# Kernel optimization log

Hardware: AMD Instinct MI355X
Metric: run time of the kernel (lower is better)

Reference implementation:

```python
import jax, jax.numpy as jnp
import numpy as np

B, C, H, W = 8, 512, 64, 64
CQ = C // 8  # query/key projection dim


def setup_inputs() -> dict:
    key = jax.random.key(0)
    ks = jax.random.split(key, 8)
    s = 0.02
    return {
        "x": jax.random.normal(ks[0], (B, C, H, W), dtype=jnp.float32),
        "Wq": jax.random.normal(ks[1], (CQ, C), dtype=jnp.float32) * s,
        "bq": jax.random.normal(ks[2], (CQ,), dtype=jnp.float32) * s,
        "Wk": jax.random.normal(ks[3], (CQ, C), dtype=jnp.float32) * s,
        "bk": jax.random.normal(ks[4], (CQ,), dtype=jnp.float32) * s,
        "Wv": jax.random.normal(ks[5], (C, C), dtype=jnp.float32) * s,
        "bv": jax.random.normal(ks[6], (C,), dtype=jnp.float32) * s,
        "gamma": jax.random.normal(ks[7], (1,), dtype=jnp.float32) * 0.1,
    }


def reference(x, Wq, bq, Wk, bk, Wv, bv, gamma):
    b, c, h, w = x.shape
    n = h * w
    xf = x.reshape(b, c, n)                                  # [B,C,N]
    # 1x1 convs == per-pixel linear maps over channels
    q = jnp.einsum('dc,bcn->bdn', Wq, xf) + bq[:, None]       # [B,CQ,N]
    k = jnp.einsum('dc,bcn->bdn', Wk, xf) + bk[:, None]       # [B,CQ,N]
    v = jnp.einsum('dc,bcn->bdn', Wv, xf) + bv[:, None]       # [B,C,N]
    # attention[b, i, j] = softmax_j( q_i . k_j )
    attn = jax.nn.softmax(jnp.einsum('bdn,bdm->bnm', q, k), axis=-1)  # [B,N,N]
    # out[b, c, i] = sum_j v[b, c, j] * attn[b, i, j]
    out = jnp.einsum('bcj,bij->bci', v, attn).reshape(b, c, h, w)
    return gamma[0] * out + x
```

## Files before the change

kernel.cpp:

```cpp
#include <hip/hip_runtime.h>
#include <hip/hip_bf16.h>

#define BB 8
#define CC 512
#define NN 4096
#define CQ 64

typedef __bf16 bf16;
typedef __bf16 bf16x4 __attribute__((ext_vector_type(4)));
typedef __bf16 bf16x8 __attribute__((ext_vector_type(8)));
typedef float f32x4 __attribute__((ext_vector_type(4)));

__device__ __forceinline__ f32x4 mfma16(bf16x8 a, bf16x8 b, f32x4 c) {
    return __builtin_amdgcn_mfma_f32_16x16x32_bf16(a, b, c, 0, 0, 0);
}

#define BAR_LDS()                                            \
    do {                                                     \
        asm volatile("s_waitcnt lgkmcnt(0)" ::: "memory");   \
        __builtin_amdgcn_s_barrier();                        \
    } while (0)


__global__ __launch_bounds__(256) void k_transpose(const float* __restrict__ x,
                                                   bf16* __restrict__ xTt) {
    __shared__ float tile[64][65];
    const int b  = blockIdx.z;
    const int c0 = blockIdx.y * 64;
    const int n0 = blockIdx.x * 64;
    const int t  = threadIdx.x;

    const float* xp = x + ((size_t)b * CC + c0) * NN + n0;
#pragma unroll
    for (int r = 0; r < 16; ++r) {
        int c = r * 4 + (t >> 6);
        int n = t & 63;
        tile[c][n] = xp[(size_t)c * NN + n];
    }
    __syncthreads();
#pragma unroll
    for (int r = 0; r < 16; ++r) {
        int nl = r * 4 + (t >> 6);
        int cl = t & 63;
        size_t off = ((size_t)(b * 256 + (n0 >> 4) + (nl >> 4)) * 16 + (c0 >> 5) + (cl >> 5)) * 512
                   + (nl & 15) * 32 + (cl & 31);
        xTt[off] = (bf16)tile[cl][nl];
    }
}

__global__ __launch_bounds__(256) void k_castw(const float* __restrict__ Wq,
                                               const float* __restrict__ Wk,
                                               const float* __restrict__ Wv,
                                               bf16* __restrict__ Wqt,
                                               bf16* __restrict__ Wkt,
                                               bf16* __restrict__ Wvt) {
    int i = blockIdx.x * 256 + threadIdx.x;
    const int nqk = CQ * CC;
    const float* src;
    bf16* dst;
    int j;
    if (i < nqk) {
        src = Wq; dst = Wqt; j = i;
    } else if (i < 2 * nqk) {
        src = Wk; dst = Wkt; j = i - nqk;
    } else if (i < 2 * nqk + CC * CC) {
        src = Wv; dst = Wvt; j = i - 2 * nqk;
    } else {
        return;
    }
    int d = j >> 9;
    int c = j & 511;
    size_t off = ((size_t)(d >> 4) * 16 + (c >> 5)) * 512 + (d & 15) * 32 + (c & 31);
    dst[off] = (bf16)src[j];
}

__global__ __launch_bounds__(256) void k_proj_qk(const bf16* __restrict__ xTt,
                                                 const bf16* __restrict__ Wqt,
                                                 const bf16* __restrict__ Wkt,
                                                 const float* __restrict__ bq,
                                                 const float* __restrict__ bk,
                                                 bf16* __restrict__ qTt,
                                                 bf16* __restrict__ kTt) {
    const int b  = blockIdx.y;
    const int nt = blockIdx.x * 4 + (threadIdx.x >> 6);
    const int l  = threadIdx.x & 63;
    const int l15 = l & 15, lq = l >> 4;
    const int loff = l15 * 32 + lq * 8;

    f32x4 acc[8];
#pragma unroll
    for (int dt = 0; dt < 4; ++dt) {
        float bvq = bq[dt * 16 + l15];
        float bvk = bk[dt * 16 + l15];
        acc[dt]     = (f32x4){bvq, bvq, bvq, bvq};
        acc[4 + dt] = (f32x4){bvk, bvk, bvk, bvk};
    }

    const bf16* ap = xTt + ((size_t)(b * 256 + nt) * 16) * 512 + loff;
#pragma unroll 2
    for (int ct = 0; ct < 16; ++ct) {
        bf16x8 a = *(const bf16x8*)(ap + (size_t)ct * 512);
#pragma unroll
        for (int dt = 0; dt < 4; ++dt) {
            bf16x8 fq = *(const bf16x8*)(Wqt + ((size_t)dt * 16 + ct) * 512 + loff);
            acc[dt] = mfma16(a, fq, acc[dt]);
        }
#pragma unroll
        for (int dt = 0; dt < 4; ++dt) {
            bf16x8 fk = *(const bf16x8*)(Wkt + ((size_t)dt * 16 + ct) * 512 + loff);
            acc[4 + dt] = mfma16(a, fk, acc[4 + dt]);
        }
    }
#pragma unroll
    for (int dt = 0; dt < 4; ++dt) {
#pragma unroll
        for (int r = 0; r < 4; ++r) {
            size_t off = ((size_t)(b * 256 + nt) * 2 + (dt >> 1)) * 512
                       + (lq * 4 + r) * 32 + (dt & 1) * 16 + l15;
            qTt[off] = (bf16)acc[dt][r];
            kTt[off] = (bf16)acc[4 + dt][r];
        }
    }
}

__global__ __launch_bounds__(256, 2) void k_proj_v(const bf16* __restrict__ xTt,
                                                   const bf16* __restrict__ Wvt,
                                                   const float* __restrict__ bv,
                                                   bf16* __restrict__ vt) {
    const int b  = blockIdx.y;
    const int bx = blockIdx.x;
    const int w  = threadIdx.x >> 6;
    const int l  = threadIdx.x & 63;
    const int l15 = l & 15, lq = l >> 4;
    const int loff = l15 * 32 + lq * 8;

    f32x4 acc[8][4];
#pragma unroll
    for (int dt = 0; dt < 8; ++dt) {
        f32x4 binit;
#pragma unroll
        for (int r = 0; r < 4; ++r) binit[r] = bv[(w * 8 + dt) * 16 + lq * 4 + r];
#pragma unroll
        for (int nt = 0; nt < 4; ++nt) acc[dt][nt] = binit;
    }

    const bf16* ap = Wvt + ((size_t)(w * 8) * 16) * 512 + loff;
    const bf16* bp = xTt + ((size_t)(b * 256 + bx * 4) * 16) * 512 + loff;
#pragma unroll 1
    for (int ct = 0; ct < 16; ++ct) {
        bf16x8 bxf[4];
#pragma unroll
        for (int nt = 0; nt < 4; ++nt)
            bxf[nt] = *(const bf16x8*)(bp + ((size_t)nt * 16 + ct) * 512);
#pragma unroll
        for (int dt = 0; dt < 8; ++dt) {
            bf16x8 aW = *(const bf16x8*)(ap + ((size_t)dt * 16 + ct) * 512);
#pragma unroll
            for (int nt = 0; nt < 4; ++nt)
                acc[dt][nt] = mfma16(aW, bxf[nt], acc[dt][nt]);
        }
    }
#pragma unroll
    for (int dt = 0; dt < 8; ++dt) {
#pragma unroll
        for (int nt = 0; nt < 4; ++nt) {
#pragma unroll
            for (int r = 0; r < 4; ++r) {
                size_t off = ((size_t)(b * 32 + w * 8 + dt) * 128 + bx * 2 + (nt >> 1)) * 512
                           + (lq * 4 + r) * 32 + (nt & 1) * 16 + l15;
                vt[off] = (bf16)acc[dt][nt][r];
            }
        }
    }
}

__global__ __launch_bounds__(512, 2) void k_attn(const bf16* __restrict__ qTt,
                                                 const bf16* __restrict__ kTt,
                                                 const bf16* __restrict__ vt,
                                                 const float* __restrict__ x,
                                                 const float* __restrict__ gamma,
                                                 float* __restrict__ out) {
    __shared__ bf16  Pl[2][8][1024];
    __shared__ bf16  Kl[2][8][512];
    __shared__ float Ll[8][16];

    const int b  = blockIdx.x & 7;
    const int i0 = (blockIdx.x >> 3) * 128;
    const int t  = threadIdx.x;
    const int w  = t >> 6;
    const int l  = t & 63;
    const int l15 = l & 15, lq = l >> 4;
    const int loff = l15 * 32 + lq * 8;

    const f32x4 zero4 = {0.f, 0.f, 0.f, 0.f};

    const bf16* kb = kTt + (size_t)b * 256 * 2 * 512;
    const bf16* qb = qTt + (size_t)b * 256 * 2 * 512;
    const bf16* vb = vt + ((size_t)b * 32 + w * 4) * 128 * 512 + loff;

    bf16x8 qa0, qa1;
    {
        const bf16* qp = qb + ((size_t)((i0 >> 4) + w) * 2) * 512 + loff;
        qa0 = *(const bf16x8*)qp;
        qa1 = *(const bf16x8*)(qp + 512);
    }

    f32x4 acc[4][8];
#pragma unroll
    for (int ct = 0; ct < 4; ++ct)
#pragma unroll
        for (int it = 0; it < 8; ++it) acc[ct][it] = zero4;
    float lsum = 0.f;

    bf16x8 kcur;
    {
        bf16x8 k0 = *(const bf16x8*)(kb + (size_t)w * 512 + loff);
        *(bf16x8*)&Kl[0][w][l * 8] = k0;
        kcur = *(const bf16x8*)(kb + (size_t)(8 + w) * 512 + loff);
    }
    BAR_LDS();

#pragma unroll 2
    for (int jb = 0; jb < NN / 64; ++jb) {
        const int buf = jb & 1;

        bf16x8 va[4][2];
#pragma unroll
        for (int ct = 0; ct < 4; ++ct)
#pragma unroll
            for (int h = 0; h < 2; ++h)
                va[ct][h] = *(const bf16x8*)(vb + ((size_t)ct * 128 + jb * 2 + h) * 512);

        bf16x8 knxt;
        {
            const int jk = (jb + 2) & (NN / 64 - 1);
            knxt = *(const bf16x8*)(kb + ((size_t)jk * 8 + w) * 512 + loff);
        }

        bf16x8 ka[8];
#pragma unroll
        for (int q = 0; q < 8; ++q)
            ka[q] = *(const bf16x8*)&Kl[buf][q][l * 8];

        f32x4 st[4];
#pragma unroll
        for (int jt = 0; jt < 4; ++jt) {
            f32x4 s = mfma16(ka[jt * 2], qa0, zero4);
            st[jt] = mfma16(ka[jt * 2 + 1], qa1, s);
        }

        *(bf16x8*)&Kl[buf ^ 1][w][l * 8] = kcur;
        kcur = knxt;

#pragma unroll
        for (int jt = 0; jt < 4; ++jt) {
            float p0 = __expf(st[jt][0]);
            float p1 = __expf(st[jt][1]);
            float p2 = __expf(st[jt][2]);
            float p3 = __expf(st[jt][3]);
            lsum += (p0 + p1) + (p2 + p3);
            bf16x4 pk = {(bf16)p0, (bf16)p1, (bf16)p2, (bf16)p3};
            int g = jt * 2 + (lq >> 1);
            *(bf16x4*)&Pl[buf][w][g * 128 + l15 * 8 + (lq & 1) * 4] = pk;
        }

        BAR_LDS();

        __builtin_amdgcn_s_setprio(1);
        bf16x8 pA = *(const bf16x8*)&Pl[buf][0][l * 8];
        bf16x8 pB = *(const bf16x8*)&Pl[buf][0][512 + l * 8];
#pragma unroll
        for (int it = 0; it < 8; ++it) {
            bf16x8 nA, nB;
            if (it < 7) {
                nA = *(const bf16x8*)&Pl[buf][it + 1][l * 8];
                nB = *(const bf16x8*)&Pl[buf][it + 1][512 + l * 8];
            }
            acc[0][it] = mfma16(va[0][0], pA, acc[0][it]);
            acc[1][it] = mfma16(va[1][0], pA, acc[1][it]);
            acc[2][it] = mfma16(va[2][0], pA, acc[2][it]);
            acc[3][it] = mfma16(va[3][0], pA, acc[3][it]);
            acc[0][it] = mfma16(va[0][1], pB, acc[0][it]);
            acc[1][it] = mfma16(va[1][1], pB, acc[1][it]);
            acc[2][it] = mfma16(va[2][1], pB, acc[2][it]);
            acc[3][it] = mfma16(va[3][1], pB, acc[3][it]);
            pA = nA;
            pB = nB;
        }
        __builtin_amdgcn_s_setprio(0);
    }

    lsum += __shfl_xor(lsum, 16);
    lsum += __shfl_xor(lsum, 32);
    if (l < 16) Ll[w][l] = lsum;
    __syncthreads();

    const float g = gamma[0];
    float linv[8];
#pragma unroll
    for (int it = 0; it < 8; ++it) linv[it] = 1.0f / Ll[it][l15];

#pragma unroll
    for (int ct = 0; ct < 4; ++ct) {
#pragma unroll
        for (int it = 0; it < 8; ++it) {
#pragma unroll
            for (int r = 0; r < 4; ++r) {
                int c = (w * 4 + ct) * 16 + lq * 4 + r;
                size_t idx = ((size_t)b * CC + c) * NN + i0 + it * 16 + l15;
                out[idx] = g * (acc[ct][it][r] * linv[it]) + x[idx];
            }
        }
    }
}

extern "C" void kernel_launch(void* const* d_in, const int* in_sizes, int n_in,
                              void* d_out, int out_size, void* d_ws, size_t ws_size,
                              hipStream_t stream) {
    const float* x     = (const float*)d_in[0];
    const float* Wq    = (const float*)d_in[1];
    const float* bq    = (const float*)d_in[2];
    const float* Wk    = (const float*)d_in[3];
    const float* bk    = (const float*)d_in[4];
    const float* Wv    = (const float*)d_in[5];
    const float* bv    = (const float*)d_in[6];
    const float* gamma = (const float*)d_in[7];
    float* out = (float*)d_out;

    char* p = (char*)d_ws;
    bf16* xTt = (bf16*)p; p += (size_t)BB * NN * CC * sizeof(bf16);
    bf16* qTt = (bf16*)p; p += (size_t)BB * NN * CQ * sizeof(bf16);
    bf16* kTt = (bf16*)p; p += (size_t)BB * NN * CQ * sizeof(bf16);
    bf16* vt  = (bf16*)p; p += (size_t)BB * CC * NN * sizeof(bf16);
    bf16* Wqt = (bf16*)p; p += (size_t)CQ * CC * sizeof(bf16);
    bf16* Wkt = (bf16*)p; p += (size_t)CQ * CC * sizeof(bf16);
    bf16* Wvt = (bf16*)p; p += (size_t)CC * CC * sizeof(bf16);

    k_transpose<<<dim3(NN / 64, CC / 64, BB), 256, 0, stream>>>(x, xTt);
    k_castw<<<(2 * CQ * CC + CC * CC + 255) / 256, 256, 0, stream>>>(Wq, Wk, Wv, Wqt, Wkt, Wvt);
    k_proj_qk<<<dim3(NN / 64, BB), 256, 0, stream>>>(xTt, Wqt, Wkt, bq, bk, qTt, kTt);
    k_proj_v<<<dim3(NN / 64, BB), 256, 0, stream>>>(xTt, Wvt, bv, vt);
    k_attn<<<256, 512, 0, stream>>>(qTt, kTt, vt, x, gamma, out);
}
```

Before: 211.4 us.

## Software-pipeline QK^T and exp one tile ahead, overlapping with PV MFMAs

Restructures the main attention loop so the scores and exponentials for the next key tile are computed inside the current PV MFMA loop, with a prologue handling the first tile. Each iteration now stores previously computed probabilities to LDS, issues a single barrier, then interleaves exp work with the value-probability MFMAs. This aims to hide the transcendental and LDS write latency behind matrix-core work. It drops the unroll-by-2, removes the software prefetch of P rows, and raises register pressure by keeping packed probabilities live across iterations.

```diff
diff --git a/kernel.cpp b/kernel.cpp
--- a/kernel.cpp
+++ b/kernel.cpp
@@ -220,7 +220,28 @@
     }
     BAR_LDS();
 
-#pragma unroll 2
+    bf16x4 pk4[4];
+    {
+        bf16x8 ka[8];
+#pragma unroll
+        for (int q = 0; q < 8; ++q)
+            ka[q] = *(const bf16x8*)&Kl[0][q][l * 8];
+        float rs = 0.f;
+#pragma unroll
+        for (int jt = 0; jt < 4; ++jt) {
+            f32x4 s = mfma16(ka[jt * 2], qa0, zero4);
+            s = mfma16(ka[jt * 2 + 1], qa1, s);
+            float p0 = __expf(s[0]);
+            float p1 = __expf(s[1]);
+            float p2 = __expf(s[2]);
+            float p3 = __expf(s[3]);
+            rs += (p0 + p1) + (p2 + p3);
+            pk4[jt] = (bf16x4){(bf16)p0, (bf16)p1, (bf16)p2, (bf16)p3};
+        }
+        lsum += rs;
+    }
+
+#pragma unroll 1
     for (int jb = 0; jb < NN / 64; ++jb) {
         const int buf = jb & 1;
 
@@ -231,17 +252,21 @@
             for (int h = 0; h < 2; ++h)
                 va[ct][h] = *(const bf16x8*)(vb + ((size_t)ct * 128 + jb * 2 + h) * 512);
 
-        bf16x8 knxt;
-        {
-            const int jk = (jb + 2) & (NN / 64 - 1);
-            knxt = *(const bf16x8*)(kb + ((size_t)jk * 8 + w) * 512 + loff);
-        }
-
+#pragma unroll
+        for (int jt = 0; jt < 4; ++jt) {
+            int g = jt * 2 + (lq >> 1);
+            *(bf16x4*)&Pl[buf][w][g * 128 + l15 * 8 + (lq & 1) * 4] = pk4[jt];
+        }
+
+        *(bf16x8*)&Kl[buf ^ 1][w][l * 8] = kcur;
+
+        BAR_LDS();
+
+        __builtin_amdgcn_s_setprio(1);
         bf16x8 ka[8];
 #pragma unroll
         for (int q = 0; q < 8; ++q)
-            ka[q] = *(const bf16x8*)&Kl[buf][q][l * 8];
-
+            ka[q] = *(const bf16x8*)&Kl[buf ^ 1][q][l * 8];
         f32x4 st[4];
 #pragma unroll
         for (int jt = 0; jt < 4; ++jt) {
@@ -249,33 +274,16 @@
             st[jt] = mfma16(ka[jt * 2 + 1], qa1, s);
         }
 
-        *(bf16x8*)&Kl[buf ^ 1][w][l * 8] = kcur;
-        kcur = knxt;
-
-#pragma unroll
-        for (int jt = 0; jt < 4; ++jt) {
-            float p0 = __expf(st[jt][0]);
-            float p1 = __expf(st[jt][1]);
-            float p2 = __expf(st[jt][2]);
-            float p3 = __expf(st[jt][3]);
-            lsum += (p0 + p1) + (p2 + p3);
-            bf16x4 pk = {(bf16)p0, (bf16)p1, (bf16)p2, (bf16)p3};
-            int g = jt * 2 + (lq >> 1);
-            *(bf16x4*)&Pl[buf][w][g * 128 + l15 * 8 + (lq & 1) * 4] = pk;
-        }
-
-        BAR_LDS();
-
-        __builtin_amdgcn_s_setprio(1);
-        bf16x8 pA = *(const bf16x8*)&Pl[buf][0][l * 8];
-        bf16x8 pB = *(const bf16x8*)&Pl[buf][0][512 + l * 8];
+        {
+            const int jk = (jb + 2) & (NN / 64 - 1);
+            kcur = *(const bf16x8*)(kb + ((size_t)jk * 8 + w) * 512 + loff);
+        }
+
+        float rs = 0.f;
 #pragma unroll
         for (int it = 0; it < 8; ++it) {
-            bf16x8 nA, nB;
-            if (it < 7) {
-                nA = *(const bf16x8*)&Pl[buf][it + 1][l * 8];
-                nB = *(const bf16x8*)&Pl[buf][it + 1][512 + l * 8];
-            }
+            bf16x8 pA = *(const bf16x8*)&Pl[buf][it][l * 8];
+            bf16x8 pB = *(const bf16x8*)&Pl[buf][it][512 + l * 8];
             acc[0][it] = mfma16(va[0][0], pA, acc[0][it]);
             acc[1][it] = mfma16(va[1][0], pA, acc[1][it]);
             acc[2][it] = mfma16(va[2][0], pA, acc[2][it]);
@@ -284,10 +292,18 @@
             acc[1][it] = mfma16(va[1][1], pB, acc[1][it]);
             acc[2][it] = mfma16(va[2][1], pB, acc[2][it]);
             acc[3][it] = mfma16(va[3][1], pB, acc[3][it]);
-            pA = nA;
-            pB = nB;
+            if (it < 4) {
+                float p0 = __expf(st[it][0]);
+                float p1 = __expf(st[it][1]);
+                float p2 = __expf(st[it][2]);
+                float p3 = __expf(st[it][3]);
+                rs += (p0 + p1) + (p2 + p3);
+                pk4[it] = (bf16x4){(bf16)p0, (bf16)p1, (bf16)p2, (bf16)p3};
+            }
         }
         __builtin_amdgcn_s_setprio(0);
+
+        if (jb != NN / 64 - 1) lsum += rs;
     }
 
     lsum += __shfl_xor(lsum, 16);
```

Measured after the change: 213.0 us. About the same (+0.8%).
